# Performance work log

Hardware: AMD Instinct MI355X
Metric: run time of the kernel (lower is better)

Reference implementation:

```python
import jax, jax.numpy as jnp
import numpy as np

NUM_COLUMNS = 16
INPUT_DIM = 1024
NUM_NEURONS = 256
SPARSITY = 0.05
B, S = 4, 2048


def setup_inputs() -> dict:
    key = jax.random.key(0)
    ks = jax.random.split(key, 12)
    D, C, N = INPUT_DIM, NUM_COLUMNS, NUM_NEURONS
    inp = {
        'x': jax.random.normal(ks[0], (B, S, D), dtype=jnp.float32),
        'col_emb': jax.random.normal(ks[1], (C, D), dtype=jnp.float32) * 0.02,
        'gate_w1': jax.random.normal(ks[2], (D, D // 2), dtype=jnp.float32) / np.sqrt(D),
        'gate_b1': jnp.zeros((D // 2,), dtype=jnp.float32),
        'gate_w2': jax.random.normal(ks[3], (D // 2, C), dtype=jnp.float32) / np.sqrt(D // 2),
        'gate_b2': jnp.zeros((C,), dtype=jnp.float32),
        'W_cols': jax.random.normal(ks[4], (C, D, N), dtype=jnp.float32) / np.sqrt(D),
        'b_cols': jnp.zeros((C, N), dtype=jnp.float32),
        'proj_w': jax.random.normal(ks[5], (C * N, D), dtype=jnp.float32) / np.sqrt(C * N),
        'proj_b': jnp.zeros((D,), dtype=jnp.float32),
        'ln_g': jnp.ones((D,), dtype=jnp.float32),
        'ln_b': jnp.zeros((D,), dtype=jnp.float32),
    }
    return inp


def _l2norm(v, axis=-1, eps=1e-12):
    n = jnp.sqrt(jnp.sum(v * v, axis=axis, keepdims=True))
    return v / jnp.maximum(n, eps)


def reference(x, col_emb, gate_w1, gate_b1, gate_w2, gate_b2, W_cols, b_cols,
              proj_w, proj_b, ln_g, ln_b):
    Bq, Sq, D = x.shape
    C = col_emb.shape[0]
    # --- router ---
    similarity = jnp.einsum('bsd,cd->bsc', _l2norm(x), _l2norm(col_emb))
    h = jax.nn.gelu(x @ gate_w1 + gate_b1, approximate=False)
    gate_values = jax.nn.sigmoid(h @ gate_w2 + gate_b2)
    logits = similarity + gate_values  # [B,S,C]
    k = max(1, int(C * SPARSITY))
    _, top_idx = jax.lax.top_k(logits, k)
    mask = jnp.sum(jax.nn.one_hot(top_idx, C, dtype=logits.dtype), axis=-2)  # [B,S,C]
    weights = mask * jax.nn.softmax(logits, axis=-1)
    # --- per-column compute (grouped GEMM), weighted combine ---
    cols = jax.nn.gelu(jnp.einsum('bsd,cdn->bscn', x, W_cols) + b_cols,
                       approximate=False)  # [B,S,C,N]
    cols = cols * weights[..., None]
    combined = cols.reshape(Bq, Sq, -1)  # [B,S,C*N], column-major concat order
    # --- proj + residual + layernorm ---
    y = combined @ proj_w + proj_b + x
    mu = jnp.mean(y, axis=-1, keepdims=True)
    var = jnp.mean((y - mu) ** 2, axis=-1, keepdims=True)
    out = (y - mu) * jax.lax.rsqrt(var + 1e-5) * ln_g + ln_b
    return out
```

## Files before the change

### kernel.cpp

```cpp
#include <hip/hip_runtime.h>
#include <hip/hip_bf16.h>
#include <math.h>

#define D    1024
#define C    16
#define N    256
#define TOK  8192
#define DH   512
#define RT_T 16
#define WLG  160
#define BCAP 20

using bf16x8 = __attribute__((ext_vector_type(8))) short;
using f32x4  = __attribute__((ext_vector_type(4))) float;

__device__ __forceinline__ float gelu_exact(float v) {
    return 0.5f * v * (1.0f + erff(v * 0.70710678118654752440f));
}
__device__ __forceinline__ float sigmoidf_(float z) {
    return 1.0f / (1.0f + expf(-z));
}
__device__ __forceinline__ short f2bf(float f) {
    unsigned u = __float_as_uint(f);
    unsigned r = u + 0x7FFF + ((u >> 16) & 1);
    return (short)(r >> 16);
}
__device__ __forceinline__ float bf2f(short s) {
    return __uint_as_float(((unsigned)(unsigned short)s) << 16);
}

__global__ void prep_kernel(const float* __restrict__ col_emb, float* __restrict__ cnorm) {
    const int tid = threadIdx.x;
    const int c = tid >> 4, l = tid & 15;
    float acc = 0.f;
    for (int j = 0; j < 64; ++j) {
        float v = col_emb[c * D + l + 16 * j];
        acc += v * v;
    }
    for (int off = 8; off; off >>= 1) acc += __shfl_xor(acc, off, 16);
    if (l == 0) cnorm[c] = fmaxf(sqrtf(acc), 1e-12f);
}

__global__ __launch_bounds__(256) void conv_kernel(const float* __restrict__ src,
                                                   short* __restrict__ dst, int n4) {
    int i = blockIdx.x * 256 + threadIdx.x;
    const int stride = gridDim.x * 256;
    for (; i < n4; i += stride) {
        const float4 v = ((const float4*)src)[i];
        short4 o;
        o.x = f2bf(v.x); o.y = f2bf(v.y); o.z = f2bf(v.z); o.w = f2bf(v.w);
        ((short4*)dst)[i] = o;
    }
}

__global__ __launch_bounds__(256) void tconv_kernel(const float* __restrict__ src0,
        short* __restrict__ dst0, int R, int Cc) {
    __shared__ float tile[64][65];
    const int tid = threadIdx.x;
    const size_t bofs = (size_t)blockIdx.z * R * Cc;
    const float* src = src0 + bofs;
    short* dst = dst0 + bofs;
    const int cBase = blockIdx.x * 64;
    const int rBase = blockIdx.y * 64;
    const int rr = tid >> 4;
    const int cq = (tid & 15) * 4;
    #pragma unroll
    for (int h = 0; h < 4; ++h) {
        const int r = h * 16 + rr;
        const float4 v = *(const float4*)&src[(size_t)(rBase + r) * Cc + cBase + cq];
        tile[r][cq + 0] = v.x; tile[r][cq + 1] = v.y;
        tile[r][cq + 2] = v.z; tile[r][cq + 3] = v.w;
    }
    __syncthreads();
    #pragma unroll
    for (int h = 0; h < 4; ++h) {
        const int cc = h * 16 + rr;
        short4 o;
        o.x = f2bf(tile[cq + 0][cc]);
        o.y = f2bf(tile[cq + 1][cc]);
        o.z = f2bf(tile[cq + 2][cc]);
        o.w = f2bf(tile[cq + 3][cc]);
        *(short4*)&dst[(size_t)(cBase + cc) * R + rBase + cq] = o;
    }
}

__global__ __launch_bounds__(256) void gate_mfma_kernel(
        const short* __restrict__ Ag, const short* __restrict__ BTg,
        const float* __restrict__ bias, short* __restrict__ outb) {
    __shared__ short As[64 * 64];
    __shared__ short Bs[64 * 64];
    const int tid = threadIdx.x;
    const int lane = tid & 63;
    const int wave = tid >> 6;
    const int wr = wave >> 1, wc = wave & 1;

    const int rA0 = tid >> 3;
    const int rA1 = rA0 + 32;
    const int bo  = (tid & 7) * 16;
    const size_t m0 = (size_t)blockIdx.x * 64;
    const char* gA0 = (const char*)Ag + (m0 + rA0) * (D * 2) + bo;
    const char* gA1 = (const char*)Ag + (m0 + rA1) * (D * 2) + bo;
    const size_t bbase = (size_t)blockIdx.y * 64 * (D * 2);
    const char* gB0 = (const char*)BTg + bbase + (size_t)rA0 * (D * 2) + bo;
    const char* gB1 = (const char*)BTg + bbase + (size_t)rA1 * (D * 2) + bo;
    char* const wA0 = (char*)As + rA0 * 128 + (bo ^ ((rA0 & 7) << 4));
    char* const wA1 = (char*)As + rA1 * 128 + (bo ^ ((rA1 & 7) << 4));
    char* const wB0 = (char*)Bs + rA0 * 128 + (bo ^ ((rA0 & 7) << 4));
    char* const wB1 = (char*)Bs + rA1 * 128 + (bo ^ ((rA1 & 7) << 4));

    const int mrow = wr * 32 + (lane & 15);
    const int nrow = wc * 32 + (lane & 15);
    const int kbB  = (lane >> 4) * 16;
    const int swm  = (mrow & 7) << 4;
    const int swn  = (nrow & 7) << 4;

    f32x4 acc[2][2] = {};
    for (int kk = 0; kk < D / 64; ++kk) {
        *(bf16x8*)wA0 = *(const bf16x8*)gA0;
        *(bf16x8*)wA1 = *(const bf16x8*)gA1;
        *(bf16x8*)wB0 = *(const bf16x8*)gB0;
        *(bf16x8*)wB1 = *(const bf16x8*)gB1;
        gA0 += 128; gA1 += 128; gB0 += 128; gB1 += 128;
        __syncthreads();
        #pragma unroll
        for (int ks = 0; ks < 2; ++ks) {
            bf16x8 aF[2], bF[2];
            #pragma unroll
            for (int i = 0; i < 2; ++i)
                aF[i] = *(const bf16x8*)((const char*)As + (mrow + i * 16) * 128
                                         + ((kbB + ks * 64) ^ swm));
            #pragma unroll
            for (int j = 0; j < 2; ++j)
                bF[j] = *(const bf16x8*)((const char*)Bs + (nrow + j * 16) * 128
                                         + ((kbB + ks * 64) ^ swn));
            #pragma unroll
            for (int i = 0; i < 2; ++i)
                #pragma unroll
                for (int j = 0; j < 2; ++j)
                    acc[i][j] = __builtin_amdgcn_mfma_f32_16x16x32_bf16(
                                    aF[i], bF[j], acc[i][j], 0, 0, 0);
        }
        __syncthreads();
    }
    const int crow = (lane >> 4) * 4;
    const int ccol = lane & 15;
    const int n0 = blockIdx.y * 64;
    #pragma unroll
    for (int i = 0; i < 2; ++i)
        #pragma unroll
        for (int j = 0; j < 2; ++j) {
            const int n = n0 + wc * 32 + j * 16 + ccol;
            const float bb = bias[n];
            #pragma unroll
            for (int r = 0; r < 4; ++r) {
                const int m = (int)m0 + wr * 32 + i * 16 + crow + r;
                outb[(size_t)m * DH + n] = f2bf(gelu_exact(acc[i][j][r] + bb));
            }
        }
}

template<int MODE>
__global__ __launch_bounds__(256) void mfma_tile(
        const short* __restrict__ Ag, const short* __restrict__ BTg,
        const float* __restrict__ bias, const float* __restrict__ x,
        const int* __restrict__ order, const float* __restrict__ wgt,
        const int* __restrict__ wl,
        short* __restrict__ outb, float* __restrict__ outf) {
    constexpr int KDIM = (MODE == 2) ? N : D;
    constexpr int KSTEPS = KDIM / 64;
    __shared__ short As[64 * 64];
    __shared__ short Bs[64 * 64];
    __shared__ int   tokl[64];
    __shared__ float wgl[64];

    const int e = wl[blockIdx.x];
    if (e < 0) return;
    const int col  = e >> 24;
    const int nt   = (e >> 16) & 0xFF;
    const int base = e & 0xFFFF;

    const int tid = threadIdx.x;
    const int lane = tid & 63;
    const int wave = tid >> 6;
    const int wr = wave >> 1, wc = wave & 1;

    if (tid < 64) {
        const int i = tid < nt ? tid : nt - 1;
        const int t = order[base + i];
        tokl[tid] = t;
        if (MODE == 1) wgl[tid] = wgt[t];
    }
    __syncthreads();

    const int rA0 = tid >> 3;
    const int rA1 = rA0 + 32;
    const int bo  = (tid & 7) * 16;
    const char* gA0; const char* gA1;
    if (MODE == 1) {
        gA0 = (const char*)Ag + (size_t)tokl[rA0] * (D * 2) + bo;
        gA1 = (const char*)Ag + (size_t)tokl[rA1] * (D * 2) + bo;
    } else {
        const int s0 = base + min(rA0, nt - 1);
        const int s1 = base + min(rA1, nt - 1);
        gA0 = (const char*)Ag + (size_t)s0 * (N * 2) + bo;
        gA1 = (const char*)Ag + (size_t)s1 * (N * 2) + bo;
    }
    const size_t bRowB = KDIM * 2;
    size_t bbase;
    if (MODE == 1) bbase = ((size_t)col * N + blockIdx.y * 64) * bRowB;
    else           bbase = ((size_t)col * D + blockIdx.y * 64) * bRowB;
    const char* gB0 = (const char*)BTg + bbase + (size_t)rA0 * bRowB + bo;
    const char* gB1 = (const char*)BTg + bbase + (size_t)rA1 * bRowB + bo;

    char* const wA0 = (char*)As + rA0 * 128 + (bo ^ ((rA0 & 7) << 4));
    char* const wA1 = (char*)As + rA1 * 128 + (bo ^ ((rA1 & 7) << 4));
    char* const wB0 = (char*)Bs + rA0 * 128 + (bo ^ ((rA0 & 7) << 4));
    char* const wB1 = (char*)Bs + rA1 * 128 + (bo ^ ((rA1 & 7) << 4));

    const int mrow = wr * 32 + (lane & 15);
    const int nrow = wc * 32 + (lane & 15);
    const int kbB  = (lane >> 4) * 16;
    const int swm  = (mrow & 7) << 4;
    const int swn  = (nrow & 7) << 4;

    f32x4 acc[2][2] = {};
    for (int kk = 0; kk < KSTEPS; ++kk) {
        *(bf16x8*)wA0 = *(const bf16x8*)gA0;
        *(bf16x8*)wA1 = *(const bf16x8*)gA1;
        *(bf16x8*)wB0 = *(const bf16x8*)gB0;
        *(bf16x8*)wB1 = *(const bf16x8*)gB1;
        gA0 += 128; gA1 += 128; gB0 += 128; gB1 += 128;
        __syncthreads();
        #pragma unroll
        for (int ks = 0; ks < 2; ++ks) {
            bf16x8 aF[2], bF[2];
            #pragma unroll
            for (int i = 0; i < 2; ++i)
                aF[i] = *(const bf16x8*)((const char*)As + (mrow + i * 16) * 128
                                         + ((kbB + ks * 64) ^ swm));
            #pragma unroll
            for (int j = 0; j < 2; ++j)
                bF[j] = *(const bf16x8*)((const char*)Bs + (nrow + j * 16) * 128
                                         + ((kbB + ks * 64) ^ swn));
            #pragma unroll
            for (int i = 0; i < 2; ++i)
                #pragma unroll
                for (int j = 0; j < 2; ++j)
                    acc[i][j] = __builtin_amdgcn_mfma_f32_16x16x32_bf16(
                                    aF[i], bF[j], acc[i][j], 0, 0, 0);
        }
        __syncthreads();
    }

    const int crow = (lane >> 4) * 4;
    const int ccol = lane & 15;
    if (MODE == 1) {
        const int n0 = blockIdx.y * 64;
        #pragma unroll
        for (int i = 0; i < 2; ++i)
            #pragma unroll
            for (int j = 0; j < 2; ++j) {
                const int n = n0 + wc * 32 + j * 16 + ccol;
                const float bb = bias[col * N + n];
                #pragma unroll
                for (int r = 0; r < 4; ++r) {
                    const int il = wr * 32 + i * 16 + crow + r;
                    if (il < nt) {
                        const float v = gelu_exact(acc[i][j][r] + bb) * wgl[il];
                        outb[(size_t)(base + il) * N + n] = f2bf(v);
                    }
                }
            }
    } else {
        const int n0 = blockIdx.y * 64;
        #pragma unroll
        for (int i = 0; i < 2; ++i)
            #pragma unroll
            for (int j = 0; j < 2; ++j) {
                const int dcol = n0 + wc * 32 + j * 16 + ccol;
                const float bb = bias[dcol];
                #pragma unroll
                for (int r = 0; r < 4; ++r) {
                    const int il = wr * 32 + i * 16 + crow + r;
                    if (il < nt) {
                        const size_t ofs = (size_t)tokl[il] * D + dcol;
                        outf[ofs] = acc[i][j][r] + bb + x[ofs];
                    }
                }
            }
    }
}

__global__ __launch_bounds__(256) void route_kernel(
        const float* __restrict__ x, const short* __restrict__ Hb,
        const float* __restrict__ col_emb, const float* __restrict__ cnorm,
        const float* __restrict__ w2, const float* __restrict__ b2,
        int* __restrict__ idx, float* __restrict__ wgt) {
    __shared__ float P[256][33];
    __shared__ float Q[8][33];
    __shared__ float SSW[4];
    __shared__ float FL[RT_T][34];
    const int tid = threadIdx.x;
    const int lane = tid & 63;
    const int t0 = blockIdx.x * RT_T;
    const int swz = (tid & 7) << 2;

    float4 ce[C];
    #pragma unroll
    for (int c = 0; c < C; ++c)
        ce[c] = *(const float4*)&col_emb[c * D + tid * 4];
    float w2r[2][C];
    #pragma unroll
    for (int r2 = 0; r2 < 2; ++r2)
        #pragma unroll
        for (int cq = 0; cq < 4; ++cq) {
            const float4 v = *(const float4*)&w2[(tid * 2 + r2) * C + cq * 4];
            w2r[r2][cq * 4 + 0] = v.x; w2r[r2][cq * 4 + 1] = v.y;
            w2r[r2][cq * 4 + 2] = v.z; w2r[r2][cq * 4 + 3] = v.w;
        }

    for (int ti = 0; ti < RT_T; ++ti) {
        const int t = t0 + ti;
        const float4 xv = *(const float4*)&x[(size_t)t * D + tid * 4];
        const unsigned hu = *(const unsigned*)&Hb[(size_t)t * DH + tid * 2];
        const float h0 = bf2f((short)(hu & 0xffff));
        const float h1 = bf2f((short)(hu >> 16));
        float pv[32];
        #pragma unroll
        for (int c = 0; c < C; ++c)
            pv[c] = xv.x * ce[c].x + xv.y * ce[c].y + xv.z * ce[c].z + xv.w * ce[c].w;
        #pragma unroll
        for (int c = 0; c < C; ++c)
            pv[C + c] = h0 * w2r[0][c] + h1 * w2r[1][c];
        float ssp = xv.x * xv.x + xv.y * xv.y + xv.z * xv.z + xv.w * xv.w;
        #pragma unroll
        for (int off = 32; off; off >>= 1) ssp += __shfl_xor(ssp, off);
        if (lane == 0) SSW[tid >> 6] = ssp;
        #pragma unroll
        for (int c = 0; c < 32; ++c)
            P[tid][c ^ swz] = pv[c];
        __syncthreads();
        {
            const int v = tid & 31, jj = tid >> 5;
            float s = 0.f;
            #pragma unroll
            for (int k = 0; k < 32; ++k) {
                const int row = jj * 32 + k;
                s += P[row][v ^ ((row & 7) << 2)];
            }
            Q[jj][v] = s;
        }
        __syncthreads();
        if (tid < 32) {
            float f = 0.f;
            #pragma unroll
            for (int j2 = 0; j2 < 8; ++j2) f += Q[j2][tid];
            FL[ti][tid] = f;
        } else if (tid == 32) {
            FL[ti][32] = SSW[0] + SSW[1] + SSW[2] + SSW[3];
        }
        __syncthreads();
    }

    if (tid < RT_T) {
        const int t = t0 + tid;
        const float xn = fmaxf(sqrtf(FL[tid][32]), 1e-12f);
        float logit[C];
        #pragma unroll
        for (int c = 0; c < C; ++c)
            logit[c] = FL[tid][c] / (xn * cnorm[c])
                     + sigmoidf_(FL[tid][C + c] + b2[c]);
        float mx = logit[0]; int am = 0;
        #pragma unroll
        for (int c = 1; c < C; ++c)
            if (logit[c] > mx) { mx = logit[c]; am = c; }
        float se = 0.f;
        #pragma unroll
        for (int c = 0; c < C; ++c) se += expf(logit[c] - mx);
        idx[t] = am;
        wgt[t] = 1.f / se;
    }
}

__global__ __launch_bounds__(256) void hist_kernel(const int* __restrict__ idx,
        int* __restrict__ cursor, int* __restrict__ wl) {
    __shared__ int h[C];
    const int tid = threadIdx.x;
    if (tid < C) h[tid] = 0;
    for (int i = tid; i < WLG; i += 256) wl[i] = -1;
    __syncthreads();
    for (int t = tid; t < TOK; t += 256) atomicAdd(&h[idx[t]], 1);
    __syncthreads();
    if (tid == 0) {
        int s = 0;
        int slots[8] = {0, 0, 0, 0, 0, 0, 0, 0};
        for (int c = 0; c < C; ++c) {
            cursor[c] = s;
            for (int st = 0; st < h[c]; st += 64) {
                const int ntg = min(64, h[c] - st);
                int b = c & 7;
                while (slots[b] >= BCAP) b = (b + 1) & 7;
                wl[slots[b] * 8 + b] = (c << 24) | (ntg << 16) | (s + st);
                slots[b]++;
            }
            s += h[c];
        }
    }
}

__global__ __launch_bounds__(256) void scatter_kernel(const int* __restrict__ idx,
        int* __restrict__ cursor, int* __restrict__ order) {
    __shared__ int lh[C];
    __shared__ int lbase[C];
    const int tid = threadIdx.x;
    const int t = blockIdx.x * 256 + tid;
    if (tid < C) lh[tid] = 0;
    __syncthreads();
    const int c = idx[t];
    const int p = atomicAdd(&lh[c], 1);
    __syncthreads();
    if (tid < C) lbase[tid] = atomicAdd(&cursor[tid], lh[tid]);
    __syncthreads();
    order[lbase[c] + p] = t;
}

__global__ __launch_bounds__(256) void ln_kernel(float* __restrict__ out,
        const float* __restrict__ g, const float* __restrict__ b) {
    __shared__ float wr_[4], wr2[4];
    const int t = blockIdx.x, tid = threadIdx.x;
    const float4 v = *(const float4*)&out[(size_t)t * D + tid * 4];
    float s = v.x + v.y + v.z + v.w;
    float s2 = v.x * v.x + v.y * v.y + v.z * v.z + v.w * v.w;
    for (int off = 32; off; off >>= 1) { s += __shfl_xor(s, off); s2 += __shfl_xor(s2, off); }
    if ((tid & 63) == 0) { wr_[tid >> 6] = s; wr2[tid >> 6] = s2; }
    __syncthreads();
    const float sum = wr_[0] + wr_[1] + wr_[2] + wr_[3];
    const float sum2 = wr2[0] + wr2[1] + wr2[2] + wr2[3];
    const float mu = sum * (1.f / D);
    const float var = sum2 * (1.f / D) - mu * mu;
    const float inv = rsqrtf(var + 1e-5f);
    const float4 g4 = *(const float4*)&g[tid * 4];
    const float4 b4 = *(const float4*)&b[tid * 4];
    float4 o;
    o.x = (v.x - mu) * inv * g4.x + b4.x;
    o.y = (v.y - mu) * inv * g4.y + b4.y;
    o.z = (v.z - mu) * inv * g4.z + b4.z;
    o.w = (v.w - mu) * inv * g4.w + b4.w;
    *(float4*)&out[(size_t)t * D + tid * 4] = o;
}

extern "C" void kernel_launch(void* const* d_in, const int* in_sizes, int n_in,
                              void* d_out, int out_size, void* d_ws, size_t ws_size,
                              hipStream_t stream) {
    const float* x       = (const float*)d_in[0];
    const float* col_emb = (const float*)d_in[1];
    const float* gate_w1 = (const float*)d_in[2];
    const float* gate_b1 = (const float*)d_in[3];
    const float* gate_w2 = (const float*)d_in[4];
    const float* gate_b2 = (const float*)d_in[5];
    const float* W_cols  = (const float*)d_in[6];
    const float* b_cols  = (const float*)d_in[7];
    const float* proj_w  = (const float*)d_in[8];
    const float* proj_b  = (const float*)d_in[9];
    const float* ln_g    = (const float*)d_in[10];
    const float* ln_b    = (const float*)d_in[11];
    float* out = (float*)d_out;

    char* w = (char*)d_ws;
    short* xb    = (short*)w;  w += (size_t)TOK * D * 2;
    short* Hb    = (short*)w;  w += (size_t)TOK * DH * 2;
    short* actb  = (short*)w;  w += (size_t)TOK * N * 2 + 65536;
    short* w1T   = (short*)w;  w += (size_t)DH * D * 2;
    short* WcT   = (short*)w;  w += (size_t)C * N * D * 2;
    short* pwT   = (short*)w;  w += (size_t)C * D * N * 2;
    float* wgt   = (float*)w;  w += TOK * 4;
    float* cnorm = (float*)w;  w += 64;
    int*   idx   = (int*)w;    w += TOK * 4;
    int*   order = (int*)w;    w += TOK * 4;
    int*   cursor= (int*)w;    w += 64;
    int*   wl    = (int*)w;    w += WLG * 4;

    hipLaunchKernelGGL(prep_kernel, dim3(1), dim3(256), 0, stream, col_emb, cnorm);
    hipLaunchKernelGGL(conv_kernel, dim3(2048), dim3(256), 0, stream,
                       x, xb, TOK * D / 4);
    hipLaunchKernelGGL(tconv_kernel, dim3(DH / 64, D / 64, 1), dim3(256), 0, stream,
                       gate_w1, w1T, D, DH);
    hipLaunchKernelGGL(tconv_kernel, dim3(N / 64, D / 64, C), dim3(256), 0, stream,
                       W_cols, WcT, D, N);
    hipLaunchKernelGGL(tconv_kernel, dim3(D / 64, N / 64, C), dim3(256), 0, stream,
                       proj_w, pwT, N, D);
    hipLaunchKernelGGL(gate_mfma_kernel, dim3(TOK / 64, DH / 64), dim3(256), 0, stream,
                       xb, w1T, gate_b1, Hb);
    hipLaunchKernelGGL(route_kernel, dim3(TOK / RT_T), dim3(256), 0, stream,
                       x, Hb, col_emb, cnorm, gate_w2, gate_b2, idx, wgt);
    hipLaunchKernelGGL(hist_kernel, dim3(1), dim3(256), 0, stream, idx, cursor, wl);
    hipLaunchKernelGGL(scatter_kernel, dim3(TOK / 256), dim3(256), 0, stream,
                       idx, cursor, order);
    hipLaunchKernelGGL((mfma_tile<1>), dim3(WLG, N / 64), dim3(256), 0, stream,
                       xb, WcT, b_cols, nullptr, order, wgt, wl, actb, nullptr);
    hipLaunchKernelGGL((mfma_tile<2>), dim3(WLG, D / 64), dim3(256), 0, stream,
                       actb, pwT, proj_b, x, order, wgt, wl, nullptr, out);
    hipLaunchKernelGGL(ln_kernel, dim3(TOK), dim3(256), 0, stream, out, ln_g, ln_b);
}
```

Before: 167.5 us.

## Fuse prep kernels into one launch and enlarge MFMA GEMM tiles

Merges the column-norm, x-to-bf16 conversion and the three weight transpose-converts into a single kernel that dispatches on block index, removing four launches. The gate GEMM tile grows from 64x64 to 128x64 and the grouped column and projection GEMM tiles grow to 64x128, so each wave issues 8 MFMAs per k-substep and reuses its A/B fragments more. The cost is higher register and LDS use and fewer blocks in the grid, which may lower occupancy.

```diff
diff --git a/kernel.cpp b/kernel.cpp
--- a/kernel.cpp
+++ b/kernel.cpp
@@ -29,39 +29,14 @@
     return __uint_as_float(((unsigned)(unsigned short)s) << 16);
 }
 
-__global__ void prep_kernel(const float* __restrict__ col_emb, float* __restrict__ cnorm) {
-    const int tid = threadIdx.x;
-    const int c = tid >> 4, l = tid & 15;
-    float acc = 0.f;
-    for (int j = 0; j < 64; ++j) {
-        float v = col_emb[c * D + l + 16 * j];
-        acc += v * v;
-    }
-    for (int off = 8; off; off >>= 1) acc += __shfl_xor(acc, off, 16);
-    if (l == 0) cnorm[c] = fmaxf(sqrtf(acc), 1e-12f);
-}
-
-__global__ __launch_bounds__(256) void conv_kernel(const float* __restrict__ src,
-                                                   short* __restrict__ dst, int n4) {
-    int i = blockIdx.x * 256 + threadIdx.x;
-    const int stride = gridDim.x * 256;
-    for (; i < n4; i += stride) {
-        const float4 v = ((const float4*)src)[i];
-        short4 o;
-        o.x = f2bf(v.x); o.y = f2bf(v.y); o.z = f2bf(v.z); o.w = f2bf(v.w);
-        ((short4*)dst)[i] = o;
-    }
-}
-
-__global__ __launch_bounds__(256) void tconv_kernel(const float* __restrict__ src0,
-        short* __restrict__ dst0, int R, int Cc) {
-    __shared__ float tile[64][65];
-    const int tid = threadIdx.x;
-    const size_t bofs = (size_t)blockIdx.z * R * Cc;
+__device__ __forceinline__ void tconv_body(const float* __restrict__ src0,
+        short* __restrict__ dst0, int R, int Cc, int bx, int by, int bz,
+        float (*tile)[65], int tid) {
+    const size_t bofs = (size_t)bz * R * Cc;
     const float* src = src0 + bofs;
     short* dst = dst0 + bofs;
-    const int cBase = blockIdx.x * 64;
-    const int rBase = blockIdx.y * 64;
+    const int cBase = bx * 64;
+    const int rBase = by * 64;
     const int rr = tid >> 4;
     const int cq = (tid & 15) * 4;
     #pragma unroll
@@ -84,57 +59,100 @@
     }
 }
 
+__global__ __launch_bounds__(256) void prep_all_kernel(
+        const float* __restrict__ x, const float* __restrict__ col_emb,
+        const float* __restrict__ gate_w1, const float* __restrict__ W_cols,
+        const float* __restrict__ proj_w,
+        short* __restrict__ xb, short* __restrict__ w1T,
+        short* __restrict__ WcT, short* __restrict__ pwT,
+        float* __restrict__ cnorm) {
+    __shared__ float tile[64][65];
+    const int b = blockIdx.x;
+    const int tid = threadIdx.x;
+    if (b == 0) {
+        const int c = tid >> 4, l = tid & 15;
+        float acc = 0.f;
+        for (int j = 0; j < 64; ++j) {
+            float v = col_emb[c * D + l + 16 * j];
+            acc += v * v;
+        }
+        for (int off = 8; off; off >>= 1) acc += __shfl_xor(acc, off, 16);
+        if (l == 0) cnorm[c] = fmaxf(sqrtf(acc), 1e-12f);
+    } else if (b < 2049) {
+        const int base = (b - 1) * 1024;
+        #pragma unroll
+        for (int h = 0; h < 4; ++h) {
+            const int i = base + h * 256 + tid;
+            const float4 v = ((const float4*)x)[i];
+            short4 o;
+            o.x = f2bf(v.x); o.y = f2bf(v.y); o.z = f2bf(v.z); o.w = f2bf(v.w);
+            ((short4*)xb)[i] = o;
+        }
+    } else if (b < 2177) {
+        const int idx = b - 2049;
+        tconv_body(gate_w1, w1T, D, DH, idx & 7, idx >> 3, 0, tile, tid);
+    } else if (b < 3201) {
+        const int idx = b - 2177;
+        tconv_body(W_cols, WcT, D, N, idx & 3, (idx >> 2) & 15, idx >> 6, tile, tid);
+    } else {
+        const int idx = b - 3201;
+        tconv_body(proj_w, pwT, N, D, idx & 15, (idx >> 4) & 3, idx >> 6, tile, tid);
+    }
+}
+
 __global__ __launch_bounds__(256) void gate_mfma_kernel(
         const short* __restrict__ Ag, const short* __restrict__ BTg,
         const float* __restrict__ bias, short* __restrict__ outb) {
-    __shared__ short As[64 * 64];
+    __shared__ short As[128 * 64];
     __shared__ short Bs[64 * 64];
     const int tid = threadIdx.x;
     const int lane = tid & 63;
     const int wave = tid >> 6;
     const int wr = wave >> 1, wc = wave & 1;
 
-    const int rA0 = tid >> 3;
-    const int rA1 = rA0 + 32;
-    const int bo  = (tid & 7) * 16;
-    const size_t m0 = (size_t)blockIdx.x * 64;
-    const char* gA0 = (const char*)Ag + (m0 + rA0) * (D * 2) + bo;
-    const char* gA1 = (const char*)Ag + (m0 + rA1) * (D * 2) + bo;
-    const size_t bbase = (size_t)blockIdx.y * 64 * (D * 2);
-    const char* gB0 = (const char*)BTg + bbase + (size_t)rA0 * (D * 2) + bo;
-    const char* gB1 = (const char*)BTg + bbase + (size_t)rA1 * (D * 2) + bo;
-    char* const wA0 = (char*)As + rA0 * 128 + (bo ^ ((rA0 & 7) << 4));
-    char* const wA1 = (char*)As + rA1 * 128 + (bo ^ ((rA1 & 7) << 4));
-    char* const wB0 = (char*)Bs + rA0 * 128 + (bo ^ ((rA0 & 7) << 4));
-    char* const wB1 = (char*)Bs + rA1 * 128 + (bo ^ ((rA1 & 7) << 4));
-
-    const int mrow = wr * 32 + (lane & 15);
-    const int nrow = wc * 32 + (lane & 15);
-    const int kbB  = (lane >> 4) * 16;
-    const int swm  = (mrow & 7) << 4;
-    const int swn  = (nrow & 7) << 4;
-
-    f32x4 acc[2][2] = {};
+    const int rS = tid >> 3;
+    const int bo = (tid & 7) * 16;
+    const size_t m0 = (size_t)blockIdx.x * 128;
+    const int n0 = blockIdx.y * 64;
+
+    const char* gA = (const char*)Ag + (m0 + rS) * (D * 2) + bo;
+    const char* gB = (const char*)BTg + ((size_t)(n0 + rS)) * (D * 2) + bo;
+
+    const int mrow = lane & 15;
+    const int kb0 = (lane >> 4) * 16;
+
+    f32x4 acc[4][2] = {};
     for (int kk = 0; kk < D / 64; ++kk) {
-        *(bf16x8*)wA0 = *(const bf16x8*)gA0;
-        *(bf16x8*)wA1 = *(const bf16x8*)gA1;
-        *(bf16x8*)wB0 = *(const bf16x8*)gB0;
-        *(bf16x8*)wB1 = *(const bf16x8*)gB1;
-        gA0 += 128; gA1 += 128; gB0 += 128; gB1 += 128;
+        #pragma unroll
+        for (int h = 0; h < 4; ++h) {
+            const int r = rS + 32 * h;
+            *(bf16x8*)((char*)As + r * 128 + (bo ^ ((r & 7) << 4))) =
+                *(const bf16x8*)(gA + (size_t)(32 * h) * (D * 2));
+        }
+        #pragma unroll
+        for (int h = 0; h < 2; ++h) {
+            const int r = rS + 32 * h;
+            *(bf16x8*)((char*)Bs + r * 128 + (bo ^ ((r & 7) << 4))) =
+                *(const bf16x8*)(gB + (size_t)(32 * h) * (D * 2));
+        }
+        gA += 128; gB += 128;
         __syncthreads();
         #pragma unroll
         for (int ks = 0; ks < 2; ++ks) {
-            bf16x8 aF[2], bF[2];
-            #pragma unroll
-            for (int i = 0; i < 2; ++i)
-                aF[i] = *(const bf16x8*)((const char*)As + (mrow + i * 16) * 128
-                                         + ((kbB + ks * 64) ^ swm));
-            #pragma unroll
-            for (int j = 0; j < 2; ++j)
-                bF[j] = *(const bf16x8*)((const char*)Bs + (nrow + j * 16) * 128
-                                         + ((kbB + ks * 64) ^ swn));
-            #pragma unroll
-            for (int i = 0; i < 2; ++i)
+            const int kb = kb0 + ks * 64;
+            bf16x8 aF[4], bF[2];
+            #pragma unroll
+            for (int i = 0; i < 4; ++i) {
+                const int m = wr * 64 + i * 16 + mrow;
+                aF[i] = *(const bf16x8*)((const char*)As + m * 128 + (kb ^ ((m & 7) << 4)));
+            }
+            #pragma unroll
+            for (int j = 0; j < 2; ++j) {
+                const int n = wc * 32 + j * 16 + mrow;
+                bF[j] = *(const bf16x8*)((const char*)Bs + n * 128 + (kb ^ ((n & 7) << 4)));
+            }
+            #pragma unroll
+            for (int i = 0; i < 4; ++i)
                 #pragma unroll
                 for (int j = 0; j < 2; ++j)
                     acc[i][j] = __builtin_amdgcn_mfma_f32_16x16x32_bf16(
@@ -144,16 +162,15 @@
     }
     const int crow = (lane >> 4) * 4;
     const int ccol = lane & 15;
-    const int n0 = blockIdx.y * 64;
     #pragma unroll
-    for (int i = 0; i < 2; ++i)
+    for (int i = 0; i < 4; ++i)
         #pragma unroll
         for (int j = 0; j < 2; ++j) {
             const int n = n0 + wc * 32 + j * 16 + ccol;
             const float bb = bias[n];
             #pragma unroll
             for (int r = 0; r < 4; ++r) {
-                const int m = (int)m0 + wr * 32 + i * 16 + crow + r;
+                const int m = (int)m0 + wr * 64 + i * 16 + crow + r;
                 outb[(size_t)m * DH + n] = f2bf(gelu_exact(acc[i][j][r] + bb));
             }
         }
@@ -169,7 +186,7 @@
     constexpr int KDIM = (MODE == 2) ? N : D;
     constexpr int KSTEPS = KDIM / 64;
     __shared__ short As[64 * 64];
-    __shared__ short Bs[64 * 64];
+    __shared__ short Bs[128 * 64];
     __shared__ int   tokl[64];
     __shared__ float wgl[64];
 
@@ -183,6 +200,7 @@
     const int lane = tid & 63;
     const int wave = tid >> 6;
     const int wr = wave >> 1, wc = wave & 1;
+    const int n0 = blockIdx.y * 128;
 
     if (tid < 64) {
         const int i = tid < nt ? tid : nt - 1;
@@ -192,60 +210,60 @@
     }
     __syncthreads();
 
-    const int rA0 = tid >> 3;
-    const int rA1 = rA0 + 32;
-    const int bo  = (tid & 7) * 16;
+    const int rS = tid >> 3;
+    const int bo = (tid & 7) * 16;
     const char* gA0; const char* gA1;
     if (MODE == 1) {
-        gA0 = (const char*)Ag + (size_t)tokl[rA0] * (D * 2) + bo;
-        gA1 = (const char*)Ag + (size_t)tokl[rA1] * (D * 2) + bo;
+        gA0 = (const char*)Ag + (size_t)tokl[rS] * (D * 2) + bo;
+        gA1 = (const char*)Ag + (size_t)tokl[rS + 32] * (D * 2) + bo;
     } else {
-        const int s0 = base + min(rA0, nt - 1);
-        const int s1 = base + min(rA1, nt - 1);
+        const int s0 = base + min(rS, nt - 1);
+        const int s1 = base + min(rS + 32, nt - 1);
         gA0 = (const char*)Ag + (size_t)s0 * (N * 2) + bo;
         gA1 = (const char*)Ag + (size_t)s1 * (N * 2) + bo;
     }
     const size_t bRowB = KDIM * 2;
     size_t bbase;
-    if (MODE == 1) bbase = ((size_t)col * N + blockIdx.y * 64) * bRowB;
-    else           bbase = ((size_t)col * D + blockIdx.y * 64) * bRowB;
-    const char* gB0 = (const char*)BTg + bbase + (size_t)rA0 * bRowB + bo;
-    const char* gB1 = (const char*)BTg + bbase + (size_t)rA1 * bRowB + bo;
-
-    char* const wA0 = (char*)As + rA0 * 128 + (bo ^ ((rA0 & 7) << 4));
-    char* const wA1 = (char*)As + rA1 * 128 + (bo ^ ((rA1 & 7) << 4));
-    char* const wB0 = (char*)Bs + rA0 * 128 + (bo ^ ((rA0 & 7) << 4));
-    char* const wB1 = (char*)Bs + rA1 * 128 + (bo ^ ((rA1 & 7) << 4));
-
-    const int mrow = wr * 32 + (lane & 15);
-    const int nrow = wc * 32 + (lane & 15);
-    const int kbB  = (lane >> 4) * 16;
-    const int swm  = (mrow & 7) << 4;
-    const int swn  = (nrow & 7) << 4;
-
-    f32x4 acc[2][2] = {};
+    if (MODE == 1) bbase = ((size_t)col * N + n0) * bRowB;
+    else           bbase = ((size_t)col * D + n0) * bRowB;
+    const char* gB = (const char*)BTg + bbase + (size_t)rS * bRowB + bo;
+
+    const int mrow = lane & 15;
+    const int kb0 = (lane >> 4) * 16;
+
+    f32x4 acc[2][4] = {};
     for (int kk = 0; kk < KSTEPS; ++kk) {
-        *(bf16x8*)wA0 = *(const bf16x8*)gA0;
-        *(bf16x8*)wA1 = *(const bf16x8*)gA1;
-        *(bf16x8*)wB0 = *(const bf16x8*)gB0;
-        *(bf16x8*)wB1 = *(const bf16x8*)gB1;
-        gA0 += 128; gA1 += 128; gB0 += 128; gB1 += 128;
+        {
+            const int r0 = rS, r1 = rS + 32;
+            *(bf16x8*)((char*)As + r0 * 128 + (bo ^ ((r0 & 7) << 4))) = *(const bf16x8*)gA0;
+            *(bf16x8*)((char*)As + r1 * 128 + (bo ^ ((r1 & 7) << 4))) = *(const bf16x8*)gA1;
+        }
+        #pragma unroll
+        for (int h = 0; h < 4; ++h) {
+            const int r = rS + 32 * h;
+            *(bf16x8*)((char*)Bs + r * 128 + (bo ^ ((r & 7) << 4))) =
+                *(const bf16x8*)(gB + (size_t)(32 * h) * bRowB);
+        }
+        gA0 += 128; gA1 += 128; gB += 128;
         __syncthreads();
         #pragma unroll
         for (int ks = 0; ks < 2; ++ks) {
-            bf16x8 aF[2], bF[2];
-            #pragma unroll
-            for (int i = 0; i < 2; ++i)
-                aF[i] = *(const bf16x8*)((const char*)As + (mrow + i * 16) * 128
-                                         + ((kbB + ks * 64) ^ swm));
-            #pragma unroll
-            for (int j = 0; j < 2; ++j)
-                bF[j] = *(const bf16x8*)((const char*)Bs + (nrow + j * 16) * 128
-                                         + ((kbB + ks * 64) ^ swn));
+            const int kb = kb0 + ks * 64;
+            bf16x8 aF[2], bF[4];
+            #pragma unroll
+            for (int i = 0; i < 2; ++i) {
+                const int m = wr * 32 + i * 16 + mrow;
+                aF[i] = *(const bf16x8*)((const char*)As + m * 128 + (kb ^ ((m & 7) << 4)));
+            }
+            #pragma unroll
+            for (int j = 0; j < 4; ++j) {
+                const int n = wc * 64 + j * 16 + mrow;
+                bF[j] = *(const bf16x8*)((const char*)Bs + n * 128 + (kb ^ ((n & 7) << 4)));
+            }
             #pragma unroll
             for (int i = 0; i < 2; ++i)
                 #pragma unroll
-                for (int j = 0; j < 2; ++j)
+                for (int j = 0; j < 4; ++j)
                     acc[i][j] = __builtin_amdgcn_mfma_f32_16x16x32_bf16(
                                     aF[i], bF[j], acc[i][j], 0, 0, 0);
         }
@@ -255,12 +273,11 @@
     const int crow = (lane >> 4) * 4;
     const int ccol = lane & 15;
     if (MODE == 1) {
-        const int n0 = blockIdx.y * 64;
         #pragma unroll
         for (int i = 0; i < 2; ++i)
             #pragma unroll
-            for (int j = 0; j < 2; ++j) {
-                const int n = n0 + wc * 32 + j * 16 + ccol;
+            for (int j = 0; j < 4; ++j) {
+                const int n = n0 + wc * 64 + j * 16 + ccol;
                 const float bb = bias[col * N + n];
                 #pragma unroll
                 for (int r = 0; r < 4; ++r) {
@@ -272,12 +289,11 @@
                 }
             }
     } else {
-        const int n0 = blockIdx.y * 64;
         #pragma unroll
         for (int i = 0; i < 2; ++i)
             #pragma unroll
-            for (int j = 0; j < 2; ++j) {
-                const int dcol = n0 + wc * 32 + j * 16 + ccol;
+            for (int j = 0; j < 4; ++j) {
+                const int dcol = n0 + wc * 64 + j * 16 + ccol;
                 const float bb = bias[dcol];
                 #pragma unroll
                 for (int r = 0; r < 4; ++r) {
@@ -480,25 +496,19 @@
     int*   cursor= (int*)w;    w += 64;
     int*   wl    = (int*)w;    w += WLG * 4;
 
-    hipLaunchKernelGGL(prep_kernel, dim3(1), dim3(256), 0, stream, col_emb, cnorm);
-    hipLaunchKernelGGL(conv_kernel, dim3(2048), dim3(256), 0, stream,
-                       x, xb, TOK * D / 4);
-    hipLaunchKernelGGL(tconv_kernel, dim3(DH / 64, D / 64, 1), dim3(256), 0, stream,
-                       gate_w1, w1T, D, DH);
-    hipLaunchKernelGGL(tconv_kernel, dim3(N / 64, D / 64, C), dim3(256), 0, stream,
-                       W_cols, WcT, D, N);
-    hipLaunchKernelGGL(tconv_kernel, dim3(D / 64, N / 64, C), dim3(256), 0, stream,
-                       proj_w, pwT, N, D);
-    hipLaunchKernelGGL(gate_mfma_kernel, dim3(TOK / 64, DH / 64), dim3(256), 0, stream,
+    hipLaunchKernelGGL(prep_all_kernel, dim3(4225), dim3(256), 0, stream,
+                       x, col_emb, gate_w1, W_cols, proj_w,
+                       xb, w1T, WcT, pwT, cnorm);
+    hipLaunchKernelGGL(gate_mfma_kernel, dim3(TOK / 128, DH / 64), dim3(256), 0, stream,
                        xb, w1T, gate_b1, Hb);
     hipLaunchKernelGGL(route_kernel, dim3(TOK / RT_T), dim3(256), 0, stream,
                        x, Hb, col_emb, cnorm, gate_w2, gate_b2, idx, wgt);
     hipLaunchKernelGGL(hist_kernel, dim3(1), dim3(256), 0, stream, idx, cursor, wl);
     hipLaunchKernelGGL(scatter_kernel, dim3(TOK / 256), dim3(256), 0, stream,
                        idx, cursor, order);
-    hipLaunchKernelGGL((mfma_tile<1>), dim3(WLG, N / 64), dim3(256), 0, stream,
+    hipLaunchKernelGGL((mfma_tile<1>), dim3(WLG, N / 128), dim3(256), 0, stream,
                        xb, WcT, b_cols, nullptr, order, wgt, wl, actb, nullptr);
-    hipLaunchKernelGGL((mfma_tile<2>), dim3(WLG, D / 64), dim3(256), 0, stream,
+    hipLaunchKernelGGL((mfma_tile<2>), dim3(WLG, D / 128), dim3(256), 0, stream,
                        actb, pwT, proj_b, x, order, wgt, wl, nullptr, out);
     hipLaunchKernelGGL(ln_kernel, dim3(TOK), dim3(256), 0, stream, out, ln_g, ln_b);
 }
```

Result: slower. 175.0 us (+4.4%).
